# Performance work log

Hardware: AMD Instinct MI355X
Metric: run time of the kernel (lower is better)

## Reference

```python
import jax, jax.numpy as jnp
import numpy as np

Q_MAX = 255.0   # 2**8 - 1
SMOOTH = 0.995
NUM_CLUSTERS = 8


def setup_inputs() -> dict:
    key = jax.random.key(0)
    ks = jax.random.split(key, 7)
    B, C, H, W = 64, 256, 64, 64
    Cs = 64  # _make_divisible(256 // 4, 8)
    x = jax.random.normal(ks[0], (B, C, H, W), dtype=jnp.float32)
    w1 = jax.random.normal(ks[1], (Cs, C), dtype=jnp.float32) * 0.05
    b1 = jax.random.normal(ks[2], (Cs,), dtype=jnp.float32) * 0.05
    w2 = jax.random.normal(ks[3], (C, Cs), dtype=jnp.float32) * 0.05
    b2 = jax.random.normal(ks[4], (C,), dtype=jnp.float32) * 0.05
    # act_range[c] = (min, max); sort so min <= max
    ar = jax.random.normal(ks[5], (NUM_CLUSTERS, 2), dtype=jnp.float32) * 3.0
    act_range = jnp.sort(ar, axis=1)
    # sorted cluster id per batch sample (batch_cluster run-length encoding)
    sample_cluster = jnp.sort(jax.random.randint(ks[6], (B,), 0, NUM_CLUSTERS, dtype=jnp.int32))
    return {"x": x, "w1": w1, "b1": b1, "w2": w2, "b2": b2,
            "act_range": act_range, "sample_cluster": sample_cluster}


def _hardsigmoid(v):
    return jnp.clip(v / 6.0 + 0.5, 0.0, 1.0)


def reference(x, w1, b1, w2, b2, act_range, sample_cluster):
    B = x.shape[0]
    # --- SE scale: global avg pool + two 1x1 convs + hardsigmoid ---
    pooled = jnp.mean(x, axis=(2, 3))                     # [B, C]
    h = jax.nn.relu(jnp.einsum('bc,sc->bs', pooled, w1) + b1)   # [B, Cs]
    v = jnp.einsum('bs,cs->bc', h, w2) + b2               # [B, C]
    scale = _hardsigmoid(v)
    out = scale[:, :, None, None] * x                     # [B, C, H, W]

    # --- per-cluster EMA range update (all clusters in EMA mode) ---
    flat = out.reshape(B, -1)
    smin = jnp.min(flat, axis=1)                          # per-sample min
    smax = jnp.max(flat, axis=1)
    cmin = jax.ops.segment_min(smin, sample_cluster, num_segments=NUM_CLUSTERS)
    cmax = jax.ops.segment_max(smax, sample_cluster, num_segments=NUM_CLUSTERS)
    new_min = act_range[:, 0] * SMOOTH + cmin * (1.0 - SMOOTH)
    new_max = act_range[:, 1] * SMOOTH + cmax * (1.0 - SMOOTH)

    # --- per-cluster fake quantization (affine, asymmetric, q_max=255) ---
    s = (new_max - new_min) / Q_MAX                       # [NC]
    z = -jnp.round(new_min / s)                           # [NC]
    ss = s[sample_cluster][:, None, None, None]           # [B,1,1,1]
    zz = z[sample_cluster][:, None, None, None]
    q = jnp.clip(jnp.round(out / ss + zz), 0.0, Q_MAX)
    fq = (q - zz) * ss
    # STE: forward = fq, backward = identity
    out_q = out + jax.lax.stop_gradient(fq - out)
    return out_q
```

## Files before the change

### kernel.cpp

```cpp
#include <hip/hip_runtime.h>

#define B_  64
#define C_  256
#define CS  64
#define NC  8
#define HW  4096
#define BC  16384

typedef float v4f __attribute__((ext_vector_type(4)));


__global__ __launch_bounds__(256) void k_reduce(const float* __restrict__ x,
    float* __restrict__ sumb, float* __restrict__ minb, float* __restrict__ maxb){
  int p = blockIdx.x;
  int t = threadIdx.x;
  const float4* base = (const float4*)(x + (size_t)p * HW);
  float s = 0.f, mn = INFINITY, mx = -INFINITY;
  #pragma unroll
  for (int k = 0; k < 4; k++){
    float4 v = base[t + 256 * k];
    s += (v.x + v.y) + (v.z + v.w);
    mn = fminf(mn, fminf(fminf(v.x, v.y), fminf(v.z, v.w)));
    mx = fmaxf(mx, fmaxf(fmaxf(v.x, v.y), fmaxf(v.z, v.w)));
  }
  #pragma unroll
  for (int off = 1; off < 64; off <<= 1){
    s  += __shfl_xor(s, off, 64);
    mn  = fminf(mn, __shfl_xor(mn, off, 64));
    mx  = fmaxf(mx, __shfl_xor(mx, off, 64));
  }
  __shared__ float ls[4], lmn[4], lmx[4];
  int w = t >> 6;
  if ((t & 63) == 0){ ls[w] = s; lmn[w] = mn; lmx[w] = mx; }
  __syncthreads();
  if (t == 0){
    sumb[p] = ls[0] + ls[1] + ls[2] + ls[3];
    minb[p] = fminf(fminf(lmn[0], lmn[1]), fminf(lmn[2], lmn[3]));
    maxb[p] = fmaxf(fmaxf(lmx[0], lmx[1]), fmaxf(lmx[2], lmx[3]));
  }
}

__global__ __launch_bounds__(256) void k_mlp(
    const float* __restrict__ sumb, const float* __restrict__ minb, const float* __restrict__ maxb,
    const float* __restrict__ w1, const float* __restrict__ b1,
    const float* __restrict__ w2, const float* __restrict__ b2,
    float* __restrict__ scaleb, float* __restrict__ sminb, float* __restrict__ smaxb){
  int b = blockIdx.x;
  int t = threadIdx.x;
  __shared__ float s_pool[C_];
  __shared__ float s_h[CS];
  __shared__ float lmn[4], lmx[4];

  s_pool[t] = sumb[b * C_ + t] * (1.0f / 4096.0f);
  __syncthreads();

  if (t < CS){
    const float4* pw = (const float4*)(w1 + t * C_);
    const float4* pp = (const float4*)s_pool;
    float acc = 0.f;
    #pragma unroll
    for (int i = 0; i < 64; i++){
      float4 w = pw[i], p = pp[i];
      acc += p.x*w.x + p.y*w.y + p.z*w.z + p.w*w.w;
    }
    s_h[t] = fmaxf(acc + b1[t], 0.f);
  }
  __syncthreads();

  const float4* pw2 = (const float4*)(w2 + t * CS);
  const float4* ph  = (const float4*)s_h;
  float acc = 0.f;
  #pragma unroll
  for (int i = 0; i < 16; i++){
    float4 w = pw2[i], h = ph[i];
    acc += h.x*w.x + h.y*w.y + h.z*w.z + h.w*w.w;
  }
  float v = acc + b2[t];
  float sc = fminf(fmaxf(v * (1.0f / 6.0f) + 0.5f, 0.f), 1.f);
  scaleb[b * C_ + t] = sc;

  float mn = sc * minb[b * C_ + t];
  float mx = sc * maxb[b * C_ + t];
  #pragma unroll
  for (int off = 1; off < 64; off <<= 1){
    mn = fminf(mn, __shfl_xor(mn, off, 64));
    mx = fmaxf(mx, __shfl_xor(mx, off, 64));
  }
  int w = t >> 6;
  if ((t & 63) == 0){ lmn[w] = mn; lmx[w] = mx; }
  __syncthreads();
  if (t == 0){
    sminb[b] = fminf(fminf(lmn[0], lmn[1]), fminf(lmn[2], lmn[3]));
    smaxb[b] = fmaxf(fmaxf(lmx[0], lmx[1]), fmaxf(lmx[2], lmx[3]));
  }
}

__global__ __launch_bounds__(64) void k_cluster(
    const float* __restrict__ sminb, const float* __restrict__ smaxb,
    const float* __restrict__ act_range, const int* __restrict__ clus,
    float* __restrict__ ssb, float* __restrict__ zzb){
  __shared__ float s_s[NC], s_z[NC];
  int t = threadIdx.x;
  if (t < NC){
    float cm = INFINITY, cM = -INFINITY;
    for (int b = 0; b < B_; b++){
      if (clus[b] == t){ cm = fminf(cm, sminb[b]); cM = fmaxf(cM, smaxb[b]); }
    }
    float nmin = act_range[2*t]     * 0.995f + cm * 0.005f;
    float nmax = act_range[2*t + 1] * 0.995f + cM * 0.005f;
    float sv = (nmax - nmin) / 255.0f;
    s_s[t] = sv;
    s_z[t] = -rintf(nmin / sv);
  }
  __syncthreads();
  int k = clus[t];
  ssb[t] = s_s[k];
  zzb[t] = s_z[k];
}

__global__ __launch_bounds__(256) void k_quant(const float* __restrict__ x,
    const float* __restrict__ scaleb, const float* __restrict__ ssb, const float* __restrict__ zzb,
    float* __restrict__ out){
  int p = (BC - 1) - blockIdx.x;
  int b = p >> 8;
  float sc = scaleb[p];
  float ss = ssb[b];
  float zz = zzb[b];
  float inv = 1.0f / ss;
  const v4f* xin = (const v4f*)(x + (size_t)p * HW);
  v4f*       oq  = (v4f*)(out + (size_t)p * HW);
  int t = threadIdx.x;
  #pragma unroll
  for (int k = 0; k < 4; k++){
    v4f v = xin[t + 256 * k];
    float in[4] = {v.x, v.y, v.z, v.w};
    float r[4];
    #pragma unroll
    for (int i = 0; i < 4; i++){
      float o = sc * in[i];
      float q = fminf(fmaxf(rintf(__builtin_fmaf(o, inv, zz)), 0.f), 255.f);
      float f = (q - zz) * ss;
      r[i] = o + (f - o);
    }
    v4f res;
    res.x = r[0]; res.y = r[1]; res.z = r[2]; res.w = r[3];
    __builtin_nontemporal_store(res, oq + t + 256 * k);
  }
}

extern "C" void kernel_launch(void* const* d_in, const int* in_sizes, int n_in,
                              void* d_out, int out_size, void* d_ws, size_t ws_size,
                              hipStream_t stream) {
  const float* x  = (const float*)d_in[0];
  const float* w1 = (const float*)d_in[1];
  const float* b1 = (const float*)d_in[2];
  const float* w2 = (const float*)d_in[3];
  const float* b2 = (const float*)d_in[4];
  const float* ar = (const float*)d_in[5];
  const int* clus = (const int*)d_in[6];
  float* out = (float*)d_out;

  float* ws    = (float*)d_ws;
  float* sumb  = ws;
  float* minb  = ws + BC;
  float* maxb  = ws + 2 * BC;
  float* scaleb= ws + 3 * BC;
  float* ssb   = ws + 4 * BC;
  float* zzb   = ssb + B_;
  float* sminb = zzb + B_;
  float* smaxb = sminb + B_;

  hipLaunchKernelGGL(k_reduce, dim3(BC), dim3(256), 0, stream, x, sumb, minb, maxb);
  hipLaunchKernelGGL(k_mlp, dim3(B_), dim3(256), 0, stream,
                     sumb, minb, maxb, w1, b1, w2, b2, scaleb, sminb, smaxb);
  hipLaunchKernelGGL(k_cluster, dim3(1), dim3(64), 0, stream,
                     sminb, smaxb, ar, clus, ssb, zzb);
  hipLaunchKernelGGL(k_quant, dim3(BC), dim3(256), 0, stream, x, scaleb, ssb, zzb, out);
}
```

Baseline: 498.4 us.

## Fold cluster reduction into MLP via atomics and process two planes per quant block

Drops the single-block cluster kernel. Per-sample min and max are now merged into per-cluster slots inside the MLP kernel using atomicMin and atomicMax on order-preserving unsigned keys, and the reduce kernel initialises those slots. The quant kernel derives scale and zero-point itself and handles two channel planes per block, issuing nontemporal loads for both up front. This removes one launch and raises memory parallelism per thread. The cost is atomics, repeated per-block scale math, and reliance on block 0 of k_reduce initialising the slots before k_mlp runs.

```diff
diff --git a/kernel.cpp b/kernel.cpp
--- a/kernel.cpp
+++ b/kernel.cpp
@@ -10,10 +10,24 @@
 typedef float v4f __attribute__((ext_vector_type(4)));
 
 
+__device__ __forceinline__ unsigned int enc_key(float f){
+  unsigned int u = __float_as_uint(f);
+  return (u & 0x80000000u) ? ~u : (u | 0x80000000u);
+}
+__device__ __forceinline__ float dec_key(unsigned int key){
+  unsigned int u = (key & 0x80000000u) ? (key ^ 0x80000000u) : ~key;
+  return __uint_as_float(u);
+}
+
 __global__ __launch_bounds__(256) void k_reduce(const float* __restrict__ x,
-    float* __restrict__ sumb, float* __restrict__ minb, float* __restrict__ maxb){
+    float* __restrict__ sumb, float* __restrict__ minb, float* __restrict__ maxb,
+    unsigned int* __restrict__ cmin_enc, unsigned int* __restrict__ cmax_enc){
   int p = blockIdx.x;
   int t = threadIdx.x;
+  if (p == 0 && t < NC){
+    cmin_enc[t] = 0xFF800000u;
+    cmax_enc[t] = 0x007FFFFFu;
+  }
   const float4* base = (const float4*)(x + (size_t)p * HW);
   float s = 0.f, mn = INFINITY, mx = -INFINITY;
   #pragma unroll
@@ -44,7 +58,9 @@
     const float* __restrict__ sumb, const float* __restrict__ minb, const float* __restrict__ maxb,
     const float* __restrict__ w1, const float* __restrict__ b1,
     const float* __restrict__ w2, const float* __restrict__ b2,
-    float* __restrict__ scaleb, float* __restrict__ sminb, float* __restrict__ smaxb){
+    const int* __restrict__ clus,
+    float* __restrict__ scaleb,
+    unsigned int* __restrict__ cmin_enc, unsigned int* __restrict__ cmax_enc){
   int b = blockIdx.x;
   int t = threadIdx.x;
   __shared__ float s_pool[C_];
@@ -90,61 +106,67 @@
   if ((t & 63) == 0){ lmn[w] = mn; lmx[w] = mx; }
   __syncthreads();
   if (t == 0){
-    sminb[b] = fminf(fminf(lmn[0], lmn[1]), fminf(lmn[2], lmn[3]));
-    smaxb[b] = fmaxf(fmaxf(lmx[0], lmx[1]), fmaxf(lmx[2], lmx[3]));
+    float smin = fminf(fminf(lmn[0], lmn[1]), fminf(lmn[2], lmn[3]));
+    float smax = fmaxf(fmaxf(lmx[0], lmx[1]), fmaxf(lmx[2], lmx[3]));
+    int k = clus[b];
+    atomicMin(&cmin_enc[k], enc_key(smin));
+    atomicMax(&cmax_enc[k], enc_key(smax));
   }
 }
 
-__global__ __launch_bounds__(64) void k_cluster(
-    const float* __restrict__ sminb, const float* __restrict__ smaxb,
+__global__ __launch_bounds__(256) void k_quant(const float* __restrict__ x,
+    const float* __restrict__ scaleb,
+    const unsigned int* __restrict__ cmin_enc, const unsigned int* __restrict__ cmax_enc,
     const float* __restrict__ act_range, const int* __restrict__ clus,
-    float* __restrict__ ssb, float* __restrict__ zzb){
-  __shared__ float s_s[NC], s_z[NC];
+    float* __restrict__ out){
+  int p0 = (BC - 2) - 2 * (int)blockIdx.x;
+  int b  = p0 >> 8;
+  int kcl = clus[b];
+  float cm = dec_key(cmin_enc[kcl]);
+  float cM = dec_key(cmax_enc[kcl]);
+  float nmin = act_range[2*kcl]     * 0.995f + cm * 0.005f;
+  float nmax = act_range[2*kcl + 1] * 0.995f + cM * 0.005f;
+  float ss = (nmax - nmin) / 255.0f;
+  float zz = -rintf(nmin / ss);
+  float inv = 1.0f / ss;
+  float sc0 = scaleb[p0];
+  float sc1 = scaleb[p0 + 1];
+
+  const v4f* x0 = (const v4f*)(x + (size_t)p0 * HW);
+  const v4f* x1 = x0 + (HW / 4);
+  v4f* o0 = (v4f*)(out + (size_t)p0 * HW);
+  v4f* o1 = o0 + (HW / 4);
   int t = threadIdx.x;
-  if (t < NC){
-    float cm = INFINITY, cM = -INFINITY;
-    for (int b = 0; b < B_; b++){
-      if (clus[b] == t){ cm = fminf(cm, sminb[b]); cM = fmaxf(cM, smaxb[b]); }
-    }
-    float nmin = act_range[2*t]     * 0.995f + cm * 0.005f;
-    float nmax = act_range[2*t + 1] * 0.995f + cM * 0.005f;
-    float sv = (nmax - nmin) / 255.0f;
-    s_s[t] = sv;
-    s_z[t] = -rintf(nmin / sv);
-  }
-  __syncthreads();
-  int k = clus[t];
-  ssb[t] = s_s[k];
-  zzb[t] = s_z[k];
-}
 
-__global__ __launch_bounds__(256) void k_quant(const float* __restrict__ x,
-    const float* __restrict__ scaleb, const float* __restrict__ ssb, const float* __restrict__ zzb,
-    float* __restrict__ out){
-  int p = (BC - 1) - blockIdx.x;
-  int b = p >> 8;
-  float sc = scaleb[p];
-  float ss = ssb[b];
-  float zz = zzb[b];
-  float inv = 1.0f / ss;
-  const v4f* xin = (const v4f*)(x + (size_t)p * HW);
-  v4f*       oq  = (v4f*)(out + (size_t)p * HW);
-  int t = threadIdx.x;
+  v4f va[4], vb[4];
+  #pragma unroll
+  for (int k = 0; k < 4; k++) va[k] = __builtin_nontemporal_load(x0 + t + 256 * k);
+  #pragma unroll
+  for (int k = 0; k < 4; k++) vb[k] = __builtin_nontemporal_load(x1 + t + 256 * k);
+
   #pragma unroll
   for (int k = 0; k < 4; k++){
-    v4f v = xin[t + 256 * k];
-    float in[4] = {v.x, v.y, v.z, v.w};
-    float r[4];
+    v4f res;
     #pragma unroll
     for (int i = 0; i < 4; i++){
-      float o = sc * in[i];
+      float o = sc0 * va[k][i];
       float q = fminf(fmaxf(rintf(__builtin_fmaf(o, inv, zz)), 0.f), 255.f);
       float f = (q - zz) * ss;
-      r[i] = o + (f - o);
+      res[i] = o + (f - o);
     }
+    __builtin_nontemporal_store(res, o0 + t + 256 * k);
+  }
+  #pragma unroll
+  for (int k = 0; k < 4; k++){
     v4f res;
-    res.x = r[0]; res.y = r[1]; res.z = r[2]; res.w = r[3];
-    __builtin_nontemporal_store(res, oq + t + 256 * k);
+    #pragma unroll
+    for (int i = 0; i < 4; i++){
+      float o = sc1 * vb[k][i];
+      float q = fminf(fmaxf(rintf(__builtin_fmaf(o, inv, zz)), 0.f), 255.f);
+      float f = (q - zz) * ss;
+      res[i] = o + (f - o);
+    }
+    __builtin_nontemporal_store(res, o1 + t + 256 * k);
   }
 }
 
@@ -165,15 +187,13 @@
   float* minb  = ws + BC;
   float* maxb  = ws + 2 * BC;
   float* scaleb= ws + 3 * BC;
-  float* ssb   = ws + 4 * BC;
-  float* zzb   = ssb + B_;
-  float* sminb = zzb + B_;
-  float* smaxb = sminb + B_;
+  unsigned int* cmin_enc = (unsigned int*)(ws + 4 * BC);
+  unsigned int* cmax_enc = cmin_enc + NC;
 
-  hipLaunchKernelGGL(k_reduce, dim3(BC), dim3(256), 0, stream, x, sumb, minb, maxb);
+  hipLaunchKernelGGL(k_reduce, dim3(BC), dim3(256), 0, stream,
+                     x, sumb, minb, maxb, cmin_enc, cmax_enc);
   hipLaunchKernelGGL(k_mlp, dim3(B_), dim3(256), 0, stream,
-                     sumb, minb, maxb, w1, b1, w2, b2, scaleb, sminb, smaxb);
-  hipLaunchKernelGGL(k_cluster, dim3(1), dim3(64), 0, stream,
-                     sminb, smaxb, ar, clus, ssb, zzb);
-  hipLaunchKernelGGL(k_quant, dim3(BC), dim3(256), 0, stream, x, scaleb, ssb, zzb, out);
+                     sumb, minb, maxb, w1, b1, w2, b2, clus, scaleb, cmin_enc, cmax_enc);
+  hipLaunchKernelGGL(k_quant, dim3(BC / 2), dim3(256), 0, stream,
+                     x, scaleb, cmin_enc, cmax_enc, ar, clus, out);
 }
```

After: 486.4 us. 2.4% less time.
